# Kernel optimization log

Measured on AMD Instinct MI355X. Metric: run time of the kernel, lower is better.

## Reference

```python
import jax, jax.numpy as jnp
import numpy as np

B, C, M = 2048, 1, 80  # M = max_object; matrices are (M+1)x(M+1)


def setup_inputs() -> dict:
    key = jax.random.key(0)
    k1, k2, k3, k4 = jax.random.split(key, 4)
    inp = {
        "input": jax.random.normal(k1, (B, C, M + 1, M + 1), dtype=jnp.float32),
        "target": jax.random.randint(k2, (B, C, M + 1, M + 1), 0, 2, dtype=jnp.int32),
        "mask0": jax.random.randint(k3, (B, C, M + 1), 0, 2, dtype=jnp.int32),
        "mask1": jax.random.randint(k4, (B, C, M + 1), 0, 2, dtype=jnp.int32),
        "outputs": 0,
        "current_fair_labels": 0,
        "next_fair_labels": 0,
    }
    return inp


def reference(input, target, mask0, mask1, outputs, current_fair_labels, next_fair_labels):
    f32 = jnp.float32
    m0 = mask0.astype(f32)[:, :, :, None]   # [B,C,M+1,1] (row mask, broadcast over cols)
    m1 = mask1.astype(f32)[:, :, None, :]   # [B,C,1,M+1] (col mask, broadcast over rows)
    mask_region = m0 * m1                    # [B,C,M+1,M+1]
    mask_region_pre = mask_region.at[:, :, M, :].set(0.0)   # zero last row
    mask_region_next = mask_region.at[:, :, :, M].set(0.0)  # zero last col
    mask_region_union = mask_region_pre * mask_region_next

    input_pre = jax.nn.softmax(mask_region_pre * input, axis=3)
    input_next = jax.nn.softmax(mask_region_next * input, axis=2)
    input_all = input_pre.at[:, :, :M, :M].set(
        jnp.maximum(input_pre, input_next)[:, :, :M, :M])

    t = target.astype(jnp.bool_).astype(f32)
    target_pre = mask_region_pre * t
    target_next = mask_region_next * t
    target_union = mask_region_union * t

    target_num = t.sum()
    n_pre = target_pre.sum()
    n_next = target_next.sum()
    n_union = target_union.sum()

    s_pre = -(target_pre * jnp.log(input_pre)).sum()
    loss_pre = jnp.where(n_pre > 0, s_pre / n_pre, s_pre)

    s_next = -(target_next * jnp.log(input_next)).sum()
    loss_next = jnp.where(n_next > 0, s_next / n_next, s_next)

    s_all = -(target_pre * jnp.log(input_all)).sum()
    loss = jnp.where((n_pre > 0) & (n_next > 0), s_all / n_pre, s_all)

    # |1 - p_pre - (1 - p_next)| == |p_next - p_pre|
    s_sim = (target_union * jnp.abs(input_next - input_pre)).sum()
    loss_similarity = jnp.where(n_union > 0, s_sim / target_num, s_sim)

    # accuracy on "pre" direction (argmax over cols, drop last row)
    idx_t_pre = jnp.argmax(target_pre, axis=3)[:, :, :-1]
    indexes_pre = jnp.argmax(input_all, axis=3)[:, :, :-1]
    mpre = mask0.astype(f32)[:, :, :-1]
    n_mpre = mpre.sum()
    s_acc_pre = ((indexes_pre == idx_t_pre).astype(f32) * mpre).sum()
    accuracy_pre = jnp.where(n_mpre > 0, s_acc_pre / n_mpre, s_acc_pre + 1.0)

    # accuracy on "next" direction (argmax over rows, drop last col)
    idx_t_next = jnp.argmax(target_next, axis=2)[:, :, :-1]
    indexes_next = jnp.argmax(input_next, axis=2)[:, :, :-1]
    mnext = mask1.astype(f32)[:, :, :-1]
    n_mnext = mnext.sum()
    s_acc_next = ((indexes_next == idx_t_next).astype(f32) * mnext).sum()
    accuracy_next = jnp.where(n_mnext > 0, s_acc_next / n_mnext, s_acc_next + 1.0)

    total = (loss_pre + loss_next + loss + loss_similarity) / 4.0
    return (loss_pre, loss_next, loss_similarity, total,
            accuracy_pre, accuracy_next, (accuracy_pre + accuracy_next) / 2.0,
            indexes_pre)
```

## Files before the change

### kernel.cpp

```cpp
#include <hip/hip_runtime.h>

#define M1 81
#define MSZ 80
#define NEL (M1 * M1)
#define NTW ((NEL + 31) / 32)
#define NACC 12
#define BIGKC 1.0e30f


__global__ __launch_bounds__(512, 8) void sst_main(
    const float* __restrict__ input,
    const int* __restrict__ target,
    const int* __restrict__ mask0,
    const int* __restrict__ mask1,
    float* __restrict__ out_idx,
    float* __restrict__ part,
    int slices)
{
    __shared__ __align__(16) float s_xraw[NEL + 4];
    __shared__ unsigned s_tb[NTW];
    __shared__ float s_m0[M1], s_m1[M1];
    __shared__ float s_kc[M1];
    __shared__ float s_invc[M1];
    __shared__ float s_pA[486];
    __shared__ float s_pC[480];
    __shared__ float s_pV[486];
    __shared__ unsigned char s_pI[486];
    __shared__ unsigned char s_pT[486];
    __shared__ unsigned char s_ci[MSZ];
    __shared__ int s_ct[MSZ];
    __shared__ unsigned s_m1w[4];
    __shared__ float s_wv[8][NACC];

    const int tid   = threadIdx.x;
    const int lane  = tid & 63;
    const int w     = tid >> 6;
    const int slice = blockIdx.x;
    const size_t base = (size_t)slice * NEL;

    float* sx = s_xraw + (slice & 3);
    const int h = (4 - (slice & 3)) & 3;

    if (tid < M1) s_m0[tid] = (float)mask0[slice * M1 + tid];
    else if (tid >= 128 && tid < 128 + M1) s_m1[tid - 128] = (float)mask1[slice * M1 + (tid - 128)];
    if (tid >= 256 && tid < 256 + MSZ) s_ct[tid - 256] = 0x7fffffff;

    float a[NACC];
#pragma unroll
    for (int k = 0; k < NACC; ++k) a[k] = 0.0f;

    const int n4 = (NEL - h) >> 2;
    const float4* in4 = (const float4*)(input + base + h);
    for (int i = tid; i < n4; i += 512)
        *(float4*)(sx + h + (i << 2)) = in4[i];
    if (tid < h) sx[tid] = input[base + tid];
    for (int i = h + (n4 << 2) + tid; i < NEL; i += 512) sx[i] = input[base + i];

    int tpre[13];
#pragma unroll
    for (int k = 0; k < 13; ++k) {
        const int i = tid + (k << 9);
        tpre[k] = (i < NEL) ? target[base + i] : 0;
    }
    __syncthreads();

    if (w == 0) {
        const unsigned long long m = __ballot(s_m1[lane] != 0.0f);
        if (lane == 0) { s_m1w[0] = (unsigned)m; s_m1w[1] = (unsigned)(m >> 32); }
    } else if (w == 1) {
        float v = 0.0f;
        if (lane < 17) v = s_m1[64 + lane];
        const unsigned long long m = __ballot(v != 0.0f);
        if (lane == 0) { s_m1w[2] = (unsigned)m; s_m1w[3] = 0u; }
    }

    if (tid < 486) {
        const int c = tid / 6, j = tid - 6 * (tid / 6);
        const int r0 = j * 13 + ((j < 3) ? j : 3);
        const int len = (j < 3) ? 14 : 13;
        const float m1c = s_m1[c];
        float cs = 0.0f, bv = -1.0f;
        int bi = r0;
        int idx = r0 * M1 + c;
        for (int i = 0; i < len; ++i, idx += M1) {
            const int r = r0 + i;
            const float z = m1c * s_m0[r] * sx[idx];
            const float e = __expf(z);
            sx[idx] = e;
            cs += e;
            if (e > bv) { bv = e; bi = r; }
        }
        s_pA[tid] = cs; s_pV[tid] = bv; s_pI[tid] = (unsigned char)bi;
    }

#pragma unroll
    for (int k = 0; k < 13; ++k) {
        const int i = tid + (k << 9);
        if (i < NEL) {
            const unsigned long long m = __ballot(tpre[k] != 0);
            if (lane == 0) {
                a[0] += (float)__popcll(m);
                const int w2 = (i >> 5) & ~1;
                s_tb[w2] = (unsigned)m;
                if (w2 + 1 < NTW) s_tb[w2 + 1] = (unsigned)(m >> 32);
            }
        }
    }
    __syncthreads();

    if (tid < 480) {
        const int r = tid / 6, j = tid - 6 * (tid / 6);
        const int c0 = j * 13 + ((j < 3) ? j : 3);
        const int len = (j < 3) ? 14 : 13;
        const int rb = r * M1 + c0;
        float rs = 0.0f;
        for (int i = 0; i < len; ++i) rs += sx[rb + i];
        s_pC[tid] = rs;
    } else {
        const int u = tid - 480;
        for (int c = u; c < M1; c += 32) {
            if (c < MSZ) {
                const int b = 6 * c;
                float cs = 0.0f;
#pragma unroll
                for (int k = 0; k < 6; ++k) cs += s_pA[b + k];
                float bv = s_pV[b]; int bi = s_pI[b];
#pragma unroll
                for (int k = 1; k < 6; ++k) {
                    const float v = s_pV[b + k];
                    if (v > bv) { bv = v; bi = s_pI[b + k]; }
                }
                s_kc[c] = __logf(cs);
                s_invc[c] = 1.0f / cs;
                s_ci[c] = (unsigned char)bi;
            } else {
                s_kc[c] = BIGKC;
                s_invc[c] = 0.0f;
            }
        }
    }
    __syncthreads();

    if (tid < 480) {
        const int r = tid / 6, j = tid - 6 * (tid / 6);
        const int c0 = j * 13 + ((j < 3) ? j : 3);
        const int len = (j < 3) ? 14 : 13;
        const int rb = r * M1;
        const int pb = 6 * r;
        const float rs = s_pC[pb] + s_pC[pb + 1] + s_pC[pb + 2]
                       + s_pC[pb + 3] + s_pC[pb + 4] + s_pC[pb + 5];
        const float lr = __logf(rs), invr = 1.0f / rs;
        const float m0f = s_m0[r];

        const int bp = rb + c0;
        const unsigned long long tw64 =
            ((unsigned long long)s_tb[(bp >> 5) + 1] << 32) | s_tb[bp >> 5];
        const int mp0 = c0 >> 5;
        const unsigned long long mw64 =
            ((unsigned long long)s_m1w[mp0 + 1] << 32) | s_m1w[mp0];
        const unsigned lenmask = (1u << len) - 1u;
        unsigned wb = (unsigned)(tw64 >> (bp & 31)) & (unsigned)(mw64 >> (c0 & 31)) & lenmask;
        if (m0f == 0.0f) wb = 0u;

        const unsigned w3 = (j == 5) ? (wb & 0x0FFFu) : wb;
        a[1] += (float)__popc(wb);
        a[2] += (float)__popc(w3);
        a[3] += (float)__popc(w3);
        const int ti = wb ? (c0 + __ffs(wb) - 1) : 127;

        float bv = -1.0f; int bi = c0;
        for (int i = 0; i < len; ++i) {
            const int c = c0 + i;
            const float val = sx[rb + c] * fmaxf(invr, s_invc[c]);
            if (val > bv) { bv = val; bi = c; }
        }
        unsigned wl = wb;
        while (wl) {
            const int b = __ffs(wl) - 1; wl &= wl - 1u;
            const int c = c0 + b;
            const float e = sx[rb + c];
            const float z = __logf(e);
            a[4] += lr - z;
            a[6] += fminf(lr, s_kc[c]) - z;
            if (c != MSZ) {
                a[5] += s_kc[c] - z;
                a[7] = fmaf(e, fabsf(s_invc[c] - invr), a[7]);
                atomicMin(&s_ct[c], r);
            }
        }
        s_pV[tid] = bv; s_pI[tid] = (unsigned char)bi; s_pT[tid] = (unsigned char)ti;
    } else if (tid < 486) {
        const int j = tid - 480;
        const int c0 = j * 13 + ((j < 3) ? j : 3);
        const int len = (j < 3) ? 14 : 13;
        const int rb = MSZ * M1;
        const float m80 = s_m0[MSZ];
        const int bp = rb + c0;
        const unsigned long long tw64 =
            ((unsigned long long)s_tb[(bp >> 5) + 1] << 32) | s_tb[bp >> 5];
        const int mp0 = c0 >> 5;
        const unsigned long long mw64 =
            ((unsigned long long)s_m1w[mp0 + 1] << 32) | s_m1w[mp0];
        const unsigned lenmask = (1u << len) - 1u;
        unsigned wb = (unsigned)(tw64 >> (bp & 31)) & (unsigned)(mw64 >> (c0 & 31)) & lenmask;
        if (m80 == 0.0f) wb = 0u;
        if (j == 5) wb &= 0x0FFFu;
        a[2] += (float)__popc(wb);
        while (wb) {
            const int b = __ffs(wb) - 1; wb &= wb - 1u;
            const int c = c0 + b;
            a[5] += s_kc[c] - __logf(sx[rb + c]);
            atomicMin(&s_ct[c], MSZ);
        }
    }
    __syncthreads();

    if (tid < MSZ) {
        const int b = 6 * tid;
        float bv = s_pV[b]; int bi = s_pI[b];
#pragma unroll
        for (int k = 1; k < 6; ++k) {
            const float v = s_pV[b + k];
            if (v > bv) { bv = v; bi = s_pI[b + k]; }
        }
        int ti = 127;
#pragma unroll
        for (int k = 0; k < 6; ++k) ti = min(ti, (int)s_pT[b + k]);
        if (ti == 127) ti = 0;
        out_idx[(size_t)slice * MSZ + tid] = (float)bi;
        const float m0f = s_m0[tid];
        a[8]  += (bi == ti) ? m0f : 0.0f;
        a[10] += m0f;
    } else if (tid >= 128 && tid < 128 + MSZ) {
        const int c = tid - 128;
        const int ctv = s_ct[c];
        const int ti = (ctv == 0x7fffffff) ? 0 : ctv;
        const int bi = (int)s_ci[c];
        const float m1c = s_m1[c];
        a[9]  += (bi == ti) ? m1c : 0.0f;
        a[11] += m1c;
    }

#pragma unroll
    for (int k = 0; k < NACC; ++k) {
        float v = a[k];
        for (int off = 32; off > 0; off >>= 1) v += __shfl_down(v, off);
        if (lane == 0) s_wv[w][k] = v;
    }
    __syncthreads();
    if (tid < NACC) {
        float s = 0.0f;
#pragma unroll
        for (int ww = 0; ww < 8; ++ww) s += s_wv[ww][tid];
        part[(size_t)tid * slices + slice] = s;
    }
}

__global__ __launch_bounds__(256) void sst_final(
    const float* __restrict__ part, int slices, float* __restrict__ out)
{
    __shared__ double s_part[4][NACC];
    const int tid = threadIdx.x;
    double l[NACC];
#pragma unroll
    for (int k = 0; k < NACC; ++k) l[k] = 0.0;
    for (int s = tid; s < slices; s += 256) {
#pragma unroll
        for (int k = 0; k < NACC; ++k) l[k] += (double)part[(size_t)k * slices + s];
    }
#pragma unroll
    for (int k = 0; k < NACC; ++k) {
        double v = l[k];
        for (int off = 32; off > 0; off >>= 1) v += __shfl_down(v, off);
        if ((tid & 63) == 0) s_part[tid >> 6][k] = v;
    }
    __syncthreads();
    if (tid == 0) {
        double g[NACC];
#pragma unroll
        for (int k = 0; k < NACC; ++k)
            g[k] = s_part[0][k] + s_part[1][k] + s_part[2][k] + s_part[3][k];
        const double tnum = g[0], npre = g[1], nnext = g[2], nunion = g[3];
        const double spre = g[4], snext = g[5], sall = g[6], ssim = g[7];
        const double accp = g[8], accn = g[9], nmp = g[10], nmn = g[11];
        const double loss_pre  = (npre > 0.0) ? spre / npre : spre;
        const double loss_next = (nnext > 0.0) ? snext / nnext : snext;
        const double loss      = (npre > 0.0 && nnext > 0.0) ? sall / npre : sall;
        const double loss_sim  = (nunion > 0.0) ? ssim / tnum : ssim;
        const double total = (loss_pre + loss_next + loss + loss_sim) * 0.25;
        const double ap = (nmp > 0.0) ? accp / nmp : accp + 1.0;
        const double an = (nmn > 0.0) ? accn / nmn : accn + 1.0;
        out[0] = (float)loss_pre;
        out[1] = (float)loss_next;
        out[2] = (float)loss_sim;
        out[3] = (float)total;
        out[4] = (float)ap;
        out[5] = (float)an;
        out[6] = (float)((ap + an) * 0.5);
    }
}

extern "C" void kernel_launch(void* const* d_in, const int* in_sizes, int n_in,
                              void* d_out, int out_size, void* d_ws, size_t ws_size,
                              hipStream_t stream) {
    const float* input  = (const float*)d_in[0];
    const int*   target = (const int*)d_in[1];
    const int*   mask0  = (const int*)d_in[2];
    const int*   mask1  = (const int*)d_in[3];
    float* out = (float*)d_out;
    float* part = (float*)d_ws;

    const int slices = in_sizes[0] / NEL;

    sst_main<<<slices, 512, 0, stream>>>(input, target, mask0, mask1, out + 7, part, slices);
    sst_final<<<1, 256, 0, stream>>>(part, slices, out);
}
```

Measured before the change: 165.3 us.

## Fuse final reduction into main kernel via last-block counter and direct LDS loads

```diff
diff --git a/kernel.cpp b/kernel.cpp
--- a/kernel.cpp
+++ b/kernel.cpp
@@ -7,15 +7,19 @@
 #define NACC 12
 #define BIGKC 1.0e30f
 
+typedef __attribute__((address_space(1))) const void* gas_t;
+typedef __attribute__((address_space(3))) void* las_t;
+
 
 __global__ __launch_bounds__(512, 8) void sst_main(
     const float* __restrict__ input,
     const int* __restrict__ target,
     const int* __restrict__ mask0,
     const int* __restrict__ mask1,
-    float* __restrict__ out_idx,
+    float* __restrict__ out,
     float* __restrict__ part,
-    int slices)
+    int slices,
+    unsigned* counter)
 {
     __shared__ __align__(16) float s_xraw[NEL + 4];
     __shared__ unsigned s_tb[NTW];
@@ -30,7 +34,8 @@
     __shared__ unsigned char s_ci[MSZ];
     __shared__ int s_ct[MSZ];
     __shared__ unsigned s_m1w[4];
-    __shared__ float s_wv[8][NACC];
+    __shared__ float s_wv[8][8][NACC];
+    __shared__ int s_lastf;
 
     const int tid   = threadIdx.x;
     const int lane  = tid & 63;
@@ -49,12 +54,19 @@
 #pragma unroll
     for (int k = 0; k < NACC; ++k) a[k] = 0.0f;
 
-    const int n4 = (NEL - h) >> 2;
+    if (tid < h) sx[tid] = input[base + tid];
     const float4* in4 = (const float4*)(input + base + h);
-    for (int i = tid; i < n4; i += 512)
-        *(float4*)(sx + h + (i << 2)) = in4[i];
-    if (tid < h) sx[tid] = input[base + tid];
-    for (int i = h + (n4 << 2) + tid; i < NEL; i += 512) sx[i] = input[base + i];
+#pragma unroll
+    for (int it = 0; it < 3; ++it) {
+        const int i = tid + (it << 9);
+        __builtin_amdgcn_global_load_lds((gas_t)(in4 + i),
+                                         (las_t)(sx + h + (i << 2)), 16, 0, 0);
+    }
+    {
+        const int i = h + 6144 + tid;
+        if (i < NEL) sx[i] = input[base + i];
+    }
+    __syncthreads();
 
     int tpre[13];
 #pragma unroll
@@ -62,7 +74,6 @@
         const int i = tid + (k << 9);
         tpre[k] = (i < NEL) ? target[base + i] : 0;
     }
-    __syncthreads();
 
     if (w == 0) {
         const unsigned long long m = __ballot(s_m1[lane] != 0.0f);
@@ -227,7 +238,7 @@
 #pragma unroll
         for (int k = 0; k < 6; ++k) ti = min(ti, (int)s_pT[b + k]);
         if (ti == 127) ti = 0;
-        out_idx[(size_t)slice * MSZ + tid] = (float)bi;
+        out[7 + (size_t)slice * MSZ + tid] = (float)bi;
         const float m0f = s_m0[tid];
         a[8]  += (bi == ti) ? m0f : 0.0f;
         a[10] += m0f;
@@ -241,18 +252,81 @@
         a[11] += m1c;
     }
 
+    float red[NACC];
 #pragma unroll
     for (int k = 0; k < NACC; ++k) {
         float v = a[k];
-        for (int off = 32; off > 0; off >>= 1) v += __shfl_down(v, off);
-        if (lane == 0) s_wv[w][k] = v;
+        v += __shfl_down(v, 32);
+        v += __shfl_down(v, 16);
+        v += __shfl_down(v, 8);
+        red[k] = v;
+    }
+    if (lane < 8) {
+#pragma unroll
+        for (int k = 0; k < NACC; ++k) s_wv[w][lane][k] = red[k];
     }
     __syncthreads();
     if (tid < NACC) {
         float s = 0.0f;
-#pragma unroll
-        for (int ww = 0; ww < 8; ++ww) s += s_wv[ww][tid];
-        part[(size_t)tid * slices + slice] = s;
+        const float* sv = (const float*)s_wv;
+#pragma unroll 8
+        for (int m = 0; m < 64; ++m) s += sv[m * NACC + tid];
+        part[(size_t)slice * NACC + tid] = s;
+    }
+
+    if (counter) {
+        if (w == 0) __threadfence();
+        __syncthreads();
+        if (tid == 0) {
+            const unsigned old = atomicAdd(counter, 1u);
+            s_lastf = (((old + 1u) % (unsigned)slices) == 0u) ? 1 : 0;
+        }
+        __syncthreads();
+        if (s_lastf) {
+            __threadfence();
+            double l[NACC];
+#pragma unroll
+            for (int k = 0; k < NACC; ++k) l[k] = 0.0;
+            for (int s = tid; s < slices; s += 512) {
+                const float* p = part + (size_t)s * NACC;
+#pragma unroll
+                for (int k = 0; k < NACC; ++k) l[k] += (double)p[k];
+            }
+            double* sd = (double*)s_xraw;
+#pragma unroll
+            for (int k = 0; k < NACC; ++k) {
+                double v = l[k];
+                for (int off = 32; off > 0; off >>= 1) v += __shfl_down(v, off);
+                if (lane == 0) sd[w * NACC + k] = v;
+            }
+            __syncthreads();
+            if (tid == 0) {
+                double g[NACC];
+#pragma unroll
+                for (int k = 0; k < NACC; ++k) {
+                    double s = 0.0;
+                    for (int ww = 0; ww < 8; ++ww) s += sd[ww * NACC + k];
+                    g[k] = s;
+                }
+                const double tnum = g[0], npre = g[1], nnext = g[2], nunion = g[3];
+                const double spre = g[4], snext = g[5], sall = g[6], ssim = g[7];
+                const double accp = g[8], accn = g[9], nmp = g[10], nmn = g[11];
+                const double loss_pre  = (npre > 0.0) ? spre / npre : spre;
+                const double loss_next = (nnext > 0.0) ? snext / nnext : snext;
+                const double loss      = (npre > 0.0 && nnext > 0.0) ? sall / npre : sall;
+                const double loss_sim  = (nunion > 0.0) ? ssim / tnum : ssim;
+                const double total = (loss_pre + loss_next + loss + loss_sim) * 0.25;
+                const double ap = (nmp > 0.0) ? accp / nmp : accp + 1.0;
+                const double an = (nmn > 0.0) ? accn / nmn : accn + 1.0;
+                out[0] = (float)loss_pre;
+                out[1] = (float)loss_next;
+                out[2] = (float)loss_sim;
+                out[3] = (float)total;
+                out[4] = (float)ap;
+                out[5] = (float)an;
+                out[6] = (float)((ap + an) * 0.5);
+            }
+        }
     }
 }
 
@@ -265,8 +339,9 @@
 #pragma unroll
     for (int k = 0; k < NACC; ++k) l[k] = 0.0;
     for (int s = tid; s < slices; s += 256) {
-#pragma unroll
-        for (int k = 0; k < NACC; ++k) l[k] += (double)part[(size_t)k * slices + s];
+        const float* p = part + (size_t)s * NACC;
+#pragma unroll
+        for (int k = 0; k < NACC; ++k) l[k] += (double)p[k];
     }
 #pragma unroll
     for (int k = 0; k < NACC; ++k) {
@@ -312,6 +387,12 @@
 
     const int slices = in_sizes[0] / NEL;
 
-    sst_main<<<slices, 512, 0, stream>>>(input, target, mask0, mask1, out + 7, part, slices);
-    sst_final<<<1, 256, 0, stream>>>(part, slices, out);
+    const size_t need = (size_t)NACC * slices * sizeof(float) + sizeof(unsigned);
+    unsigned* counter = nullptr;
+    if (ws_size >= need)
+        counter = (unsigned*)(part + (size_t)NACC * slices);
+
+    sst_main<<<slices, 512, 0, stream>>>(input, target, mask0, mask1, out, part, slices, counter);
+    if (!counter)
+        sst_final<<<1, 256, 0, stream>>>(part, slices, out);
 }
```

New measurement: 208.1 us. 25.9% more time.

## Load input columns directly into registers instead of staging through shared memory

Applied to the files above, without the earlier changes.

```diff
diff --git a/kernel.cpp b/kernel.cpp
--- a/kernel.cpp
+++ b/kernel.cpp
@@ -17,7 +17,7 @@
     float* __restrict__ part,
     int slices)
 {
-    __shared__ __align__(16) float s_xraw[NEL + 4];
+    __shared__ __align__(16) float s_x[NEL];
     __shared__ unsigned s_tb[NTW];
     __shared__ float s_m0[M1], s_m1[M1];
     __shared__ float s_kc[M1];
@@ -38,9 +38,6 @@
     const int slice = blockIdx.x;
     const size_t base = (size_t)slice * NEL;
 
-    float* sx = s_xraw + (slice & 3);
-    const int h = (4 - (slice & 3)) & 3;
-
     if (tid < M1) s_m0[tid] = (float)mask0[slice * M1 + tid];
     else if (tid >= 128 && tid < 128 + M1) s_m1[tid - 128] = (float)mask1[slice * M1 + (tid - 128)];
     if (tid >= 256 && tid < 256 + MSZ) s_ct[tid - 256] = 0x7fffffff;
@@ -49,12 +46,19 @@
 #pragma unroll
     for (int k = 0; k < NACC; ++k) a[k] = 0.0f;
 
-    const int n4 = (NEL - h) >> 2;
-    const float4* in4 = (const float4*)(input + base + h);
-    for (int i = tid; i < n4; i += 512)
-        *(float4*)(sx + h + (i << 2)) = in4[i];
-    if (tid < h) sx[tid] = input[base + tid];
-    for (int i = h + (n4 << 2) + tid; i < NEL; i += 512) sx[i] = input[base + i];
+    __syncthreads();
+
+    const bool actA = (tid < 486);
+    const int cA = tid / 6, jA = tid - 6 * (tid / 6);
+    const int r0 = jA * 13 + ((jA < 3) ? jA : 3);
+    const bool has14 = (jA < 3);
+    float v[14];
+    if (actA) {
+        const float* gp = input + base + (size_t)r0 * M1 + cA;
+#pragma unroll
+        for (int i = 0; i < 13; ++i) v[i] = gp[i * M1];
+        v[13] = gp[((jA < 5) ? 13 : 0) * M1];
+    }
 
     int tpre[13];
 #pragma unroll
@@ -62,31 +66,36 @@
         const int i = tid + (k << 9);
         tpre[k] = (i < NEL) ? target[base + i] : 0;
     }
-    __syncthreads();
 
     if (w == 0) {
         const unsigned long long m = __ballot(s_m1[lane] != 0.0f);
         if (lane == 0) { s_m1w[0] = (unsigned)m; s_m1w[1] = (unsigned)(m >> 32); }
     } else if (w == 1) {
-        float v = 0.0f;
-        if (lane < 17) v = s_m1[64 + lane];
-        const unsigned long long m = __ballot(v != 0.0f);
+        float vv = 0.0f;
+        if (lane < 17) vv = s_m1[64 + lane];
+        const unsigned long long m = __ballot(vv != 0.0f);
         if (lane == 0) { s_m1w[2] = (unsigned)m; s_m1w[3] = 0u; }
     }
 
-    if (tid < 486) {
-        const int c = tid / 6, j = tid - 6 * (tid / 6);
-        const int r0 = j * 13 + ((j < 3) ? j : 3);
-        const int len = (j < 3) ? 14 : 13;
-        const float m1c = s_m1[c];
+    if (actA) {
+        const float m1c = s_m1[cA];
         float cs = 0.0f, bv = -1.0f;
         int bi = r0;
-        int idx = r0 * M1 + c;
-        for (int i = 0; i < len; ++i, idx += M1) {
+        int idx = r0 * M1 + cA;
+#pragma unroll
+        for (int i = 0; i < 13; ++i, idx += M1) {
             const int r = r0 + i;
-            const float z = m1c * s_m0[r] * sx[idx];
+            const float z = m1c * s_m0[r] * v[i];
             const float e = __expf(z);
-            sx[idx] = e;
+            s_x[idx] = e;
+            cs += e;
+            if (e > bv) { bv = e; bi = r; }
+        }
+        if (has14) {
+            const int r = r0 + 13;
+            const float z = m1c * s_m0[r] * v[13];
+            const float e = __expf(z);
+            s_x[idx] = e;
             cs += e;
             if (e > bv) { bv = e; bi = r; }
         }
@@ -114,7 +123,7 @@
         const int len = (j < 3) ? 14 : 13;
         const int rb = r * M1 + c0;
         float rs = 0.0f;
-        for (int i = 0; i < len; ++i) rs += sx[rb + i];
+        for (int i = 0; i < len; ++i) rs += s_x[rb + i];
         s_pC[tid] = rs;
     } else {
         const int u = tid - 480;
@@ -127,8 +136,8 @@
                 float bv = s_pV[b]; int bi = s_pI[b];
 #pragma unroll
                 for (int k = 1; k < 6; ++k) {
-                    const float v = s_pV[b + k];
-                    if (v > bv) { bv = v; bi = s_pI[b + k]; }
+                    const float vv = s_pV[b + k];
+                    if (vv > bv) { bv = vv; bi = s_pI[b + k]; }
                 }
                 s_kc[c] = __logf(cs);
                 s_invc[c] = 1.0f / cs;
@@ -171,14 +180,14 @@
         float bv = -1.0f; int bi = c0;
         for (int i = 0; i < len; ++i) {
             const int c = c0 + i;
-            const float val = sx[rb + c] * fmaxf(invr, s_invc[c]);
+            const float val = s_x[rb + c] * fmaxf(invr, s_invc[c]);
             if (val > bv) { bv = val; bi = c; }
         }
         unsigned wl = wb;
         while (wl) {
             const int b = __ffs(wl) - 1; wl &= wl - 1u;
             const int c = c0 + b;
-            const float e = sx[rb + c];
+            const float e = s_x[rb + c];
             const float z = __logf(e);
             a[4] += lr - z;
             a[6] += fminf(lr, s_kc[c]) - z;
@@ -209,7 +218,7 @@
         while (wb) {
             const int b = __ffs(wb) - 1; wb &= wb - 1u;
             const int c = c0 + b;
-            a[5] += s_kc[c] - __logf(sx[rb + c]);
+            a[5] += s_kc[c] - __logf(s_x[rb + c]);
             atomicMin(&s_ct[c], MSZ);
         }
     }
@@ -220,8 +229,8 @@
         float bv = s_pV[b]; int bi = s_pI[b];
 #pragma unroll
         for (int k = 1; k < 6; ++k) {
-            const float v = s_pV[b + k];
-            if (v > bv) { bv = v; bi = s_pI[b + k]; }
+            const float vv = s_pV[b + k];
+            if (vv > bv) { bv = vv; bi = s_pI[b + k]; }
         }
         int ti = 127;
 #pragma unroll
@@ -243,9 +252,9 @@
 
 #pragma unroll
     for (int k = 0; k < NACC; ++k) {
-        float v = a[k];
-        for (int off = 32; off > 0; off >>= 1) v += __shfl_down(v, off);
-        if (lane == 0) s_wv[w][k] = v;
+        float vv = a[k];
+        for (int off = 32; off > 0; off >>= 1) vv += __shfl_down(vv, off);
+        if (lane == 0) s_wv[w][k] = vv;
     }
     __syncthreads();
     if (tid < NACC) {
```

Result: faster. 155.6 us (-5.9%).
